# Kernel optimization log

Hardware: AMD Instinct MI355X
Metric: run time of the kernel (lower is better)

## Reference

```python
import jax, jax.numpy as jnp
import numpy as np

N_HEADS = 8
EPS = 1e-5  # torch nn.LayerNorm default


def layer_norm(x, g, b):
    mu = jnp.mean(x, axis=-1, keepdims=True)
    var = jnp.var(x, axis=-1, keepdims=True)
    return (x - mu) * jax.lax.rsqrt(var + EPS) * g + b


def mha(q_in, k_in, v_in, adj, Wq, bq, Wk, bk, Wv, bv, Wo, bo, g, be):
    # Standard GL-GIN / Co-guiding MultiHeadAttention: proj -> adjacency-masked
    # scaled dot-product softmax -> out proj -> residual + LayerNorm.
    # Dropout omitted (eval mode).
    B, Lq, D = q_in.shape
    Lk = k_in.shape[1]
    d_k = Wq.shape[-1] // N_HEADS
    q = (q_in @ Wq + bq).reshape(B, Lq, N_HEADS, d_k)
    k = (k_in @ Wk + bk).reshape(B, Lk, N_HEADS, d_k)
    v = (v_in @ Wv + bv).reshape(B, Lk, N_HEADS, d_k)
    scale = jnp.asarray(1.0 / np.sqrt(d_k), q_in.dtype)
    scores = jnp.einsum('bqhd,bkhd->bhqk', q, k) * scale  # [B,H,Lq,Lk]
    neg = jnp.asarray(-1e9, scores.dtype)
    scores = jnp.where(adj[:, None, :, :] == 0, neg, scores)
    attn = jax.nn.softmax(scores, axis=-1)
    out = jnp.einsum('bhqk,bkhd->bqhd', attn, v).reshape(B, Lq, N_HEADS * d_k)
    out = out @ Wo + bo
    return layer_norm(out + q_in, g, be)


def co_guiding_forward(h_a, h_b, adj_a, adj_b, adj_ab, adj_ba,
                       Wq, bq, Wk, bk, Wv, bv, Wo, bo, ln_g, ln_b):
    # Param arrays are stacked [n_layer, 4, ...], branch order: a2a, b2b, a2b, b2a.
    input_a, input_b = h_a, h_b
    n_layer = Wq.shape[0]
    for i in range(n_layer):
        def P(j):
            return (Wq[i, j], bq[i, j], Wk[i, j], bk[i, j], Wv[i, j], bv[i, j],
                    Wo[i, j], bo[i, j], ln_g[i, j], ln_b[i, j])
        a2a = mha(h_a, h_a, h_a, adj_a, *P(0))
        b2b = mha(h_b, h_b, h_b, adj_b, *P(1))
        a2b = mha(h_b, h_a, h_a, adj_ab, *P(2))
        b2a = mha(h_a, h_b, h_b, adj_ba, *P(3))
        h_a = jax.nn.relu(a2a + b2a)
        h_b = jax.nn.relu(b2b + a2b)
    return input_a + h_a, input_b + h_b


def setup_inputs():
    key = jax.random.key(0)
    ks = jax.random.split(key, 16)
    B, N, D, L = 4, 1024, 256, 2
    f = lambda k, s: jax.random.normal(k, s, dtype=jnp.float32) * 0.05
    return {
        'h_a': jax.random.normal(ks[0], (B, N, D), dtype=jnp.float32),
        'h_b': jax.random.normal(ks[1], (B, N, D), dtype=jnp.float32),
        'adj_a': jax.random.randint(ks[2], (B, N, N), 0, 2, dtype=jnp.int32),
        'adj_b': jax.random.randint(ks[3], (B, N, N), 0, 2, dtype=jnp.int32),
        'adj_ab': jax.random.randint(ks[4], (B, N, N), 0, 2, dtype=jnp.int32),
        'adj_ba': jax.random.randint(ks[5], (B, N, N), 0, 2, dtype=jnp.int32),
        'Wq': f(ks[6], (L, 4, D, D)), 'bq': f(ks[7], (L, 4, D)),
        'Wk': f(ks[8], (L, 4, D, D)), 'bk': f(ks[9], (L, 4, D)),
        'Wv': f(ks[10], (L, 4, D, D)), 'bv': f(ks[11], (L, 4, D)),
        'Wo': f(ks[12], (L, 4, D, D)), 'bo': f(ks[13], (L, 4, D)),
        'ln_g': jnp.ones((L, 4, D), dtype=jnp.float32),
        'ln_b': jnp.zeros((L, 4, D), dtype=jnp.float32),
    }


def reference(h_a, h_b, adj_a, adj_b, adj_ab, adj_ba,
              Wq, bq, Wk, bk, Wv, bv, Wo, bo, ln_g, ln_b):
    return co_guiding_forward(h_a, h_b, adj_a, adj_b, adj_ab, adj_ba,
                              Wq, bq, Wk, bk, Wv, bv, Wo, bo, ln_g, ln_b)
```

## Files before the change

### kernel.cpp

```cpp
#include <hip/hip_runtime.h>
#include <hip/hip_bf16.h>
#include <stdint.h>


using bf16x8 = __attribute__((ext_vector_type(8))) short;
using f32x4  = __attribute__((ext_vector_type(4))) float;
using f32x16 = __attribute__((ext_vector_type(16))) float;

#define DEVI __device__ __forceinline__

DEVI uint16_t f2bf(float x) {
  uint32_t u = __float_as_uint(x);
  u += 0x7FFFu + ((u >> 16) & 1u);
  return (uint16_t)(u >> 16);
}
DEVI uint32_t packbf2(float lo, float hi) {
  union { __hip_bfloat162 h; uint32_t u; } cv;
  cv.h = __float22bfloat162_rn(make_float2(lo, hi));
  return cv.u;
}
DEVI int phi4(int m) {
  return ((m & 4) << 1) | ((m & 8) >> 1) | (m & 3);
}

__global__ __launch_bounds__(256) void wprep_k(const float* __restrict__ Wq,
                                               const float* __restrict__ Wk,
                                               const float* __restrict__ Wv,
                                               const float* __restrict__ Wo,
                                               uint16_t* __restrict__ out) {
  const int z = blockIdx.z;
  const int type = z >> 3, mat = z & 7;
  const float* W = (type == 0 ? Wq : type == 1 ? Wk : type == 2 ? Wv : Wo)
                   + (size_t)mat * 65536;
  uint16_t* o = out + (size_t)type * 524288 + (size_t)mat * 65536;
  const int r0 = blockIdx.y * 64, c0 = blockIdx.x * 64;
  __shared__ float tl[64][68];
  const int t = threadIdx.x;
  {
    const int rr = t >> 2, cb = (t & 3) * 16;
    const float* src = W + (size_t)(r0 + rr) * 256 + c0 + cb;
    #pragma unroll
    for (int q = 0; q < 4; ++q) {
      float4 v = *(const float4*)(src + q * 4);
      tl[rr][cb + q*4 + 0] = v.x; tl[rr][cb + q*4 + 1] = v.y;
      tl[rr][cb + q*4 + 2] = v.z; tl[rr][cb + q*4 + 3] = v.w;
    }
  }
  __syncthreads();
  {
    const int nn = t >> 2, kb = (t & 3) * 16;
    __align__(16) uint16_t tmp[16];
    #pragma unroll
    for (int q = 0; q < 16; ++q) tmp[q] = f2bf(tl[kb + q][nn]);
    uint16_t* dst = o + (size_t)(c0 + nn) * 256 + r0 + kb;
    *(uint4*)&dst[0] = *(uint4*)&tmp[0];
    *(uint4*)&dst[8] = *(uint4*)&tmp[8];
  }
}

__global__ __launch_bounds__(256) void cvt_k(const float* __restrict__ a,
                                             const float* __restrict__ b,
                                             uint16_t* __restrict__ oa,
                                             uint16_t* __restrict__ ob) {
  const size_t i = ((size_t)blockIdx.x * 256 + threadIdx.x) * 8;
  const float* s = blockIdx.y ? b : a;
  uint16_t* o = blockIdx.y ? ob : oa;
  const float4 f0 = *(const float4*)(s + i), f1 = *(const float4*)(s + i + 4);
  uint4 u;
  u.x = packbf2(f0.x, f0.y); u.y = packbf2(f0.z, f0.w);
  u.z = packbf2(f1.x, f1.y); u.w = packbf2(f1.z, f1.w);
  *(uint4*)(o + i) = u;
}

struct AdjArgs { const int* adj[4]; uint32_t* bits[4]; };

__global__ __launch_bounds__(256) void adjbits_k(AdjArgs a) {
  const int* adj = a.adj[blockIdx.z];
  uint32_t* bits = a.bits[blockIdx.z];
  const size_t i = (size_t)blockIdx.x * 256 + threadIdx.x;
  const int lane = threadIdx.x & 63;
  const int v = adj[i];
  unsigned long long m = __ballot(v != 0);
  if ((lane & 31) == 0) {
    const uint32_t wi = (uint32_t)(i >> 5);
    const uint32_t kw = wi & 31;
    const uint32_t q  = (wi >> 5) & 1023;
    const uint32_t bb = wi >> 15;
    bits[((bb * 32 + kw) << 10) | q] = (uint32_t)(m >> (lane & 32));
  }
}

struct GemmArgs {
  const uint16_t* A[12];
  const uint16_t* W[12];
  const float*    bias[12];
  const float*    res[12];
  void*           C[12];
  float           os[12];
  int             mode[12];
};

DEVI void stage_tile(const uint16_t* __restrict__ Ab,
                     const uint16_t* __restrict__ Wt,
                     int m0, int n0, int kk,
                     char* AsB, char* BsB, int wid, int lane) {
  #pragma unroll
  for (int i = 0; i < 2; ++i) {
    const int seg = i * 4 + wid;
    const int rl  = (seg << 4) + (lane >> 2);
    const int gs  = (lane & 3) ^ ((lane >> 3) & 3);
    const uint16_t* gA = Ab + (size_t)(m0 + rl) * 256 + kk + gs * 8;
    const uint16_t* gB = Wt + (size_t)(n0 + rl) * 256 + kk + gs * 8;
    __builtin_amdgcn_global_load_lds(
        (const __attribute__((address_space(1))) void*)gA,
        (__attribute__((address_space(3))) void*)(AsB + (seg << 10)), 16, 0, 0);
    __builtin_amdgcn_global_load_lds(
        (const __attribute__((address_space(1))) void*)gB,
        (__attribute__((address_space(3))) void*)(BsB + (seg << 10)), 16, 0, 0);
  }
}

__global__ __launch_bounds__(256) void gemm_k(GemmArgs args) {
  const int z  = blockIdx.z;
  const int m0 = blockIdx.y * 128, n0 = blockIdx.x * 128;
  const uint16_t* Ab = args.A[z];
  const uint16_t* Wt = args.W[z];
  __shared__ __align__(16) uint16_t As[2][4096];
  __shared__ __align__(16) uint16_t Bs[2][4096];
  const int t = threadIdx.x;
  const int lane = t & 63, wid = t >> 6;
  const int g = lane >> 4, c = lane & 15;
  const int gx = g ^ ((c >> 1) & 3);
  const int wm = (wid >> 1) * 64, wn = (wid & 1) * 64;
  f32x4 acc[4][4] = {};

  stage_tile(Ab, Wt, m0, n0, 0, (char*)As[0], (char*)Bs[0], wid, lane);
  __syncthreads();

  for (int ks = 0; ks < 8; ++ks) {
    const int buf = ks & 1;
    if (ks < 7)
      stage_tile(Ab, Wt, m0, n0, (ks + 1) * 32,
                 (char*)As[buf ^ 1], (char*)Bs[buf ^ 1], wid, lane);
    bf16x8 af[4], bfr[4];
    #pragma unroll
    for (int mt = 0; mt < 4; ++mt)
      af[mt]  = *(const bf16x8*)&As[buf][(wm + mt * 16 + c) * 32 + gx * 8];
    #pragma unroll
    for (int nt = 0; nt < 4; ++nt)
      bfr[nt] = *(const bf16x8*)&Bs[buf][(wn + nt * 16 + c) * 32 + gx * 8];
    #pragma unroll
    for (int mt = 0; mt < 4; ++mt)
      #pragma unroll
      for (int nt = 0; nt < 4; ++nt)
        acc[mt][nt] = __builtin_amdgcn_mfma_f32_16x16x32_bf16(af[mt], bfr[nt], acc[mt][nt], 0, 0, 0);
    if (ks < 7) __syncthreads();
  }

  const float* bias = args.bias[z];
  const float osz = args.os[z];
  const int mode = args.mode[z];
  float bv[4];
  #pragma unroll
  for (int nt = 0; nt < 4; ++nt) bv[nt] = bias[n0 + wn + nt * 16 + c];

  if (mode == 1) {
    const float* res = args.res[z];
    float* C = (float*)args.C[z];
    #pragma unroll
    for (int mt = 0; mt < 4; ++mt)
      #pragma unroll
      for (int r = 0; r < 4; ++r) {
        const int row = m0 + wm + mt * 16 + 4 * g + r;
        #pragma unroll
        for (int nt = 0; nt < 4; ++nt) {
          const int col = n0 + wn + nt * 16 + c;
          C[(size_t)row * 256 + col] = (acc[mt][nt][r] + bv[nt]) * osz + res[(size_t)row * 256 + col];
        }
      }
  } else if (mode == 2) {
    uint16_t* C = (uint16_t*)args.C[z];
    #pragma unroll
    for (int mt = 0; mt < 4; ++mt)
      #pragma unroll
      for (int r = 0; r < 4; ++r) {
        const int row = m0 + wm + mt * 16 + 4 * g + r;
        const int bb = row >> 10, n = row & 1023;
        #pragma unroll
        for (int nt = 0; nt < 4; ++nt) {
          const int col = n0 + wn + nt * 16 + c;
          const int hh = col >> 5, d = col & 31;
          C[((size_t)(bb * 8 + hh) * 1024 + n) * 32 + d] =
              f2bf((acc[mt][nt][r] + bv[nt]) * osz);
        }
      }
  } else {
    uint16_t* C = (uint16_t*)args.C[z];
    #pragma unroll
    for (int mt = 0; mt < 4; ++mt)
      #pragma unroll
      for (int r = 0; r < 4; ++r) {
        const int row = m0 + wm + mt * 16 + 4 * g + r;
        const int bb = row >> 10, n = row & 1023;
        const int nn = (n & ~15) | phi4(n & 15);
        #pragma unroll
        for (int nt = 0; nt < 4; ++nt) {
          const int col = n0 + wn + nt * 16 + c;
          const int hh = col >> 5, d = col & 31;
          C[((size_t)(bb * 8 + hh) * 32 + d) * 1024 + nn] =
              f2bf((acc[mt][nt][r] + bv[nt]) * osz);
        }
      }
  }
}

struct AttnArgs {
  const uint16_t* Q[4];
  const uint16_t* K[4];
  const uint16_t* Vt[4];
  const uint32_t* adjb[4];
  uint16_t*       O[4];
};

__global__ __launch_bounds__(256) void attn_k(AttnArgs args) {
  const int bid = blockIdx.x;
  const int qt  = bid >> 7;
  const int grp = bid & 127;
  const int bh = grp & 31, j = grp >> 5;
  const int b = bh >> 3, h = bh & 7;
  const int t = threadIdx.x, wid = t >> 6, lane = t & 63;
  const int c = lane & 31, hi = lane >> 5;
  const int qrow = qt * 128 + wid * 32 + c;

  const uint16_t* Qbh = args.Q[j] + (size_t)(b * 8 + h) * 32768;
  const uint16_t* Kbh = args.K[j] + (size_t)(b * 8 + h) * 32768;
  const uint16_t* Vp  = args.Vt[j] + ((size_t)(b * 8 + h) * 32 + c) * 1024 + hi * 8;
  const uint32_t* adjT = args.adjb[j] + (size_t)b * 32768 + qrow;

  const bf16x8 qf0 = *(const bf16x8*)&Qbh[qrow * 32 + hi * 8];
  const bf16x8 qf1 = *(const bf16x8*)&Qbh[qrow * 32 + 16 + hi * 8];

  f32x16 oacc = {};
  f32x16 cinit;
  #pragma unroll
  for (int r = 0; r < 16; ++r) cinit[r] = -12.0f;
  float l = 0.f;

  for (int k0 = 0; k0 < 1024; k0 += 32) {
    const uint32_t w = adjT[(size_t)(k0 >> 5) << 10] >> (hi * 4);
    const bf16x8 kf0 = *(const bf16x8*)&Kbh[(k0 + c) * 32 + hi * 8];
    const bf16x8 kf1 = *(const bf16x8*)&Kbh[(k0 + c) * 32 + 16 + hi * 8];
    const bf16x8 vf0 = *(const bf16x8*)(Vp + k0);
    const bf16x8 vf1 = *(const bf16x8*)(Vp + k0 + 16);

    f32x16 st = cinit;
    st = __builtin_amdgcn_mfma_f32_32x32x16_bf16(kf0, qf0, st, 0, 0, 0);
    st = __builtin_amdgcn_mfma_f32_32x32x16_bf16(kf1, qf1, st, 0, 0, 0);

    float s0 = 0.f, s1 = 0.f, s2 = 0.f, s3 = 0.f;
    #pragma unroll
    for (int r = 0; r < 16; ++r) {
      const int pos = (r & 3) + 8 * (r >> 2);
      const float bitf = (float)((w >> pos) & 1u);
      const float pv = __builtin_amdgcn_exp2f(st[r]) * bitf;
      st[r] = pv;
      if ((r & 3) == 0) s0 += pv; else if ((r & 3) == 1) s1 += pv;
      else if ((r & 3) == 2) s2 += pv; else s3 += pv;
    }
    l += (s0 + s1) + (s2 + s3);

    union PU { uint32_t u[4]; bf16x8 v; };
    PU p0, p1;
    p0.u[0] = packbf2(st[0],  st[1]);  p0.u[1] = packbf2(st[2],  st[3]);
    p0.u[2] = packbf2(st[4],  st[5]);  p0.u[3] = packbf2(st[6],  st[7]);
    p1.u[0] = packbf2(st[8],  st[9]);  p1.u[1] = packbf2(st[10], st[11]);
    p1.u[2] = packbf2(st[12], st[13]); p1.u[3] = packbf2(st[14], st[15]);

    oacc = __builtin_amdgcn_mfma_f32_32x32x16_bf16(vf0, p0.v, oacc, 0, 0, 0);
    oacc = __builtin_amdgcn_mfma_f32_32x32x16_bf16(vf1, p1.v, oacc, 0, 0, 0);

    if (__builtin_expect(__any(l > 1e18f), 0)) {
      const float ds = 0x1p-64f;
      l *= ds;
      #pragma unroll
      for (int r = 0; r < 16; ++r) { oacc[r] *= ds; cinit[r] -= 64.0f; }
    }
  }

  l += __shfl_xor(l, 32, 64);
  const float inv = 1.0f / l;
  uint16_t* O = args.O[j];
  const size_t ob = (size_t)(b * 1024 + qrow) * 256 + h * 32 + 4 * hi;
  #pragma unroll
  for (int rq = 0; rq < 4; ++rq) {
    uint2 val;
    val.x = packbf2(oacc[4*rq+0] * inv, oacc[4*rq+1] * inv);
    val.y = packbf2(oacc[4*rq+2] * inv, oacc[4*rq+3] * inv);
    *(uint2*)&O[ob + 8 * rq] = val;
  }
}

struct LnArgs {
  const float* x0; const float* x1;
  const float* g0; const float* be0;
  const float* g1; const float* be1;
  const float* addin;
  float* out;
  uint16_t* outbf;
};
struct LnBoth { LnArgs p[2]; };

__global__ __launch_bounds__(256) void ln_k(LnBoth args) {
  const LnArgs a = args.p[blockIdx.z];
  const int wid = threadIdx.x >> 6, lane = threadIdx.x & 63;
  const int row = blockIdx.x * 4 + wid;
  const size_t off = (size_t)row * 256 + lane * 4;

  const float4 x0 = *(const float4*)(a.x0 + off);
  const float4 x1 = *(const float4*)(a.x1 + off);
  float s0 = x0.x + x0.y + x0.z + x0.w;
  float s1 = x1.x + x1.y + x1.z + x1.w;
  #pragma unroll
  for (int s = 1; s < 64; s <<= 1) { s0 += __shfl_xor(s0, s, 64); s1 += __shfl_xor(s1, s, 64); }
  const float mu0 = s0 * (1.f / 256.f), mu1 = s1 * (1.f / 256.f);
  const float d0x = x0.x - mu0, d0y = x0.y - mu0, d0z = x0.z - mu0, d0w = x0.w - mu0;
  const float d1x = x1.x - mu1, d1y = x1.y - mu1, d1z = x1.z - mu1, d1w = x1.w - mu1;
  float v0 = d0x * d0x + d0y * d0y + d0z * d0z + d0w * d0w;
  float v1 = d1x * d1x + d1y * d1y + d1z * d1z + d1w * d1w;
  #pragma unroll
  for (int s = 1; s < 64; s <<= 1) { v0 += __shfl_xor(v0, s, 64); v1 += __shfl_xor(v1, s, 64); }
  const float r0 = rsqrtf(v0 * (1.f / 256.f) + 1e-5f);
  const float r1 = rsqrtf(v1 * (1.f / 256.f) + 1e-5f);

  const size_t po = (size_t)lane * 4;
  const float4 g0 = *(const float4*)(a.g0 + po), b0 = *(const float4*)(a.be0 + po);
  const float4 g1 = *(const float4*)(a.g1 + po), b1 = *(const float4*)(a.be1 + po);

  float4 y;
  y.x = fmaxf(d0x * r0 * g0.x + b0.x + d1x * r1 * g1.x + b1.x, 0.f);
  y.y = fmaxf(d0y * r0 * g0.y + b0.y + d1y * r1 * g1.y + b1.y, 0.f);
  y.z = fmaxf(d0z * r0 * g0.z + b0.z + d1z * r1 * g1.z + b1.z, 0.f);
  y.w = fmaxf(d0w * r0 * g0.w + b0.w + d1w * r1 * g1.w + b1.w, 0.f);
  if (a.addin) {
    const float4 ad = *(const float4*)(a.addin + off);
    y.x += ad.x; y.y += ad.y; y.z += ad.z; y.w += ad.w;
  }
  *(float4*)(a.out + off) = y;
  if (a.outbf) {
    uint2 vb;
    vb.x = packbf2(y.x, y.y); vb.y = packbf2(y.z, y.w);
    *(uint2*)(a.outbf + off) = vb;
  }
}

extern "C" void kernel_launch(void* const* d_in, const int* in_sizes, int n_in,
                              void* d_out, int out_size, void* d_ws, size_t ws_size,
                              hipStream_t stream) {
  (void)in_sizes; (void)n_in; (void)out_size; (void)ws_size;
  const float* h_a = (const float*)d_in[0];
  const float* h_b = (const float*)d_in[1];
  const float* bq  = (const float*)d_in[7];
  const float* bk  = (const float*)d_in[9];
  const float* bv  = (const float*)d_in[11];
  const float* bo  = (const float*)d_in[13];
  const float* lng = (const float*)d_in[14];
  const float* lnb = (const float*)d_in[15];

  const float QSC = 1.4426950408889634f * 0.17677669529663687f;

  char* ws = (char*)d_ws;
  uint16_t* WT   = (uint16_t*)ws;
  uint32_t* ADJB = (uint32_t*)(ws + (4u  << 20));
  float*    hA   = (float*)   (ws + (6u  << 20));
  float*    hB   = (float*)   (ws + (10u << 20));
  uint16_t* hAbf = (uint16_t*)(ws + (14u << 20));
  uint16_t* hBbf = (uint16_t*)(ws + (16u << 20));
  uint16_t* Qb[4]; uint16_t* Kb[4]; uint16_t* Vtb[4]; uint16_t* ATb[4]; float* MO[4];
  for (int j = 0; j < 4; ++j) {
    Qb[j]  = (uint16_t*)(ws + (18u << 20) + (size_t)j * (2u << 20));
    Kb[j]  = (uint16_t*)(ws + (26u << 20) + (size_t)j * (2u << 20));
    MO[j]  = (float*)   (ws + (18u << 20) + (size_t)j * (4u << 20));
    Vtb[j] = (uint16_t*)(ws + (34u << 20) + (size_t)j * (2u << 20));
    ATb[j] = (uint16_t*)(ws + (42u << 20) + (size_t)j * (2u << 20));
  }

  wprep_k<<<dim3(4, 4, 32), 256, 0, stream>>>(
      (const float*)d_in[6], (const float*)d_in[8],
      (const float*)d_in[10], (const float*)d_in[12], WT);
  cvt_k<<<dim3(512, 2), 256, 0, stream>>>(h_a, h_b, hAbf, hBbf);
  {
    AdjArgs aa;
    for (int j = 0; j < 4; ++j) {
      aa.adj[j]  = (const int*)d_in[2 + j];
      aa.bits[j] = ADJB + (size_t)j * 131072;
    }
    adjbits_k<<<dim3(16384, 1, 4), 256, 0, stream>>>(aa);
  }

  for (int i = 0; i < 2; ++i) {
    const float* inA = (i == 0) ? h_a : hA;
    const float* inB = (i == 0) ? h_b : hB;
    const float* qin[4]   = { inA, inB, inB, inA };
    const uint16_t* qbf[4]  = { hAbf, hBbf, hBbf, hAbf };
    const uint16_t* kvbf[4] = { hAbf, hBbf, hAbf, hBbf };

    {
      GemmArgs ga = {};
      for (int j = 0; j < 4; ++j) {
        const int mm = i * 4 + j;
        ga.A[j]     = qbf[j];  ga.W[j]     = WT + 0 * 524288 + (size_t)mm * 65536;
        ga.bias[j]  = bq + mm * 256; ga.C[j] = Qb[j];  ga.os[j] = QSC;  ga.mode[j] = 2;
        ga.A[4+j]   = kvbf[j]; ga.W[4+j]   = WT + 1 * 524288 + (size_t)mm * 65536;
        ga.bias[4+j]= bk + mm * 256; ga.C[4+j] = Kb[j]; ga.os[4+j] = 1.0f; ga.mode[4+j] = 2;
        ga.A[8+j]   = kvbf[j]; ga.W[8+j]   = WT + 2 * 524288 + (size_t)mm * 65536;
        ga.bias[8+j]= bv + mm * 256; ga.C[8+j] = Vtb[j]; ga.os[8+j] = 1.0f; ga.mode[8+j] = 3;
      }
      gemm_k<<<dim3(2, 32, 12), 256, 0, stream>>>(ga);
    }
    {
      AttnArgs at;
      for (int j = 0; j < 4; ++j) {
        at.Q[j] = Qb[j]; at.K[j] = Kb[j]; at.Vt[j] = Vtb[j];
        at.adjb[j] = ADJB + (size_t)j * 131072; at.O[j] = ATb[j];
      }
      attn_k<<<dim3(1024, 1, 1), 256, 0, stream>>>(at);
    }
    {
      GemmArgs go = {};
      for (int j = 0; j < 4; ++j) {
        const int mm = i * 4 + j;
        go.A[j] = ATb[j]; go.W[j] = WT + 3 * 524288 + (size_t)mm * 65536;
        go.bias[j] = bo + mm * 256; go.res[j] = qin[j]; go.C[j] = MO[j];
        go.os[j] = 1.0f; go.mode[j] = 1;
      }
      gemm_k<<<dim3(2, 32, 4), 256, 0, stream>>>(go);
    }
    {
      LnBoth lb;
      float* outA = (i == 1) ? (float*)d_out : hA;
      float* outB = (i == 1) ? ((float*)d_out + 1048576) : hB;
      const float* addA = (i == 1) ? h_a : nullptr;
      const float* addB = (i == 1) ? h_b : nullptr;
      uint16_t* mbA = (i == 0) ? hAbf : nullptr;
      uint16_t* mbB = (i == 0) ? hBbf : nullptr;
      lb.p[0] = { MO[0], MO[3],
                  lng + (i * 4 + 0) * 256, lnb + (i * 4 + 0) * 256,
                  lng + (i * 4 + 3) * 256, lnb + (i * 4 + 3) * 256,
                  addA, outA, mbA };
      lb.p[1] = { MO[1], MO[2],
                  lng + (i * 4 + 1) * 256, lnb + (i * 4 + 1) * 256,
                  lng + (i * 4 + 2) * 256, lnb + (i * 4 + 2) * 256,
                  addB, outB, mbB };
      ln_k<<<dim3(1024, 1, 2), 256, 0, stream>>>(lb);
    }
  }
}
```

Baseline: 228.9 us.

## Split attention keys across warps and store intermediates in bf16

The attention kernel now gives each block 64 query rows, split between two key halves handled by separate warp pairs. The halves are combined through shared memory, which doubles the grid. The running rescale guard and the -12 offset init are removed, so there is no overflow protection. The output-projection residual and result, and the layer-norm input, move from fp32 to bf16, and the fp32 hidden-state copies are dropped. This cuts memory traffic but adds extra bf16 rounding to the residual path.

```diff
diff --git a/kernel.cpp b/kernel.cpp
--- a/kernel.cpp
+++ b/kernel.cpp
@@ -19,6 +19,7 @@
   cv.h = __float22bfloat162_rn(make_float2(lo, hi));
   return cv.u;
 }
+DEVI float bf2f(uint16_t v) { return __uint_as_float((uint32_t)v << 16); }
 DEVI int phi4(int m) {
   return ((m & 4) << 1) | ((m & 8) >> 1) | (m & 3);
 }
@@ -94,7 +95,7 @@
   const uint16_t* A[12];
   const uint16_t* W[12];
   const float*    bias[12];
-  const float*    res[12];
+  const uint16_t* res[12];
   void*           C[12];
   float           os[12];
   int             mode[12];
@@ -165,8 +166,8 @@
   for (int nt = 0; nt < 4; ++nt) bv[nt] = bias[n0 + wn + nt * 16 + c];
 
   if (mode == 1) {
-    const float* res = args.res[z];
-    float* C = (float*)args.C[z];
+    const uint16_t* res = args.res[z];
+    uint16_t* C = (uint16_t*)args.C[z];
     #pragma unroll
     for (int mt = 0; mt < 4; ++mt)
       #pragma unroll
@@ -175,7 +176,8 @@
         #pragma unroll
         for (int nt = 0; nt < 4; ++nt) {
           const int col = n0 + wn + nt * 16 + c;
-          C[(size_t)row * 256 + col] = (acc[mt][nt][r] + bv[nt]) * osz + res[(size_t)row * 256 + col];
+          C[(size_t)row * 256 + col] =
+              f2bf((acc[mt][nt][r] + bv[nt]) * osz + bf2f(res[(size_t)row * 256 + col]));
         }
       }
   } else if (mode == 2) {
@@ -222,38 +224,44 @@
   uint16_t*       O[4];
 };
 
-__global__ __launch_bounds__(256) void attn_k(AttnArgs args) {
+__global__ __launch_bounds__(256, 8) void attn_k(AttnArgs args) {
   const int bid = blockIdx.x;
   const int qt  = bid >> 7;
   const int grp = bid & 127;
   const int bh = grp & 31, j = grp >> 5;
   const int b = bh >> 3, h = bh & 7;
   const int t = threadIdx.x, wid = t >> 6, lane = t & 63;
+  const int qg = wid & 1, ks = wid >> 1;
   const int c = lane & 31, hi = lane >> 5;
-  const int qrow = qt * 128 + wid * 32 + c;
+  const int hsh = hi * 4;
+  const int qrow = qt * 64 + qg * 32 + c;
 
   const uint16_t* Qbh = args.Q[j] + (size_t)(b * 8 + h) * 32768;
   const uint16_t* Kbh = args.K[j] + (size_t)(b * 8 + h) * 32768;
-  const uint16_t* Vp  = args.Vt[j] + ((size_t)(b * 8 + h) * 32 + c) * 1024 + hi * 8;
+  const uint16_t* Vbh = args.Vt[j] + ((size_t)(b * 8 + h) * 32 + c) * 1024 + hi * 8;
   const uint32_t* adjT = args.adjb[j] + (size_t)b * 32768 + qrow;
 
   const bf16x8 qf0 = *(const bf16x8*)&Qbh[qrow * 32 + hi * 8];
   const bf16x8 qf1 = *(const bf16x8*)&Qbh[qrow * 32 + 16 + hi * 8];
 
   f32x16 oacc = {};
-  f32x16 cinit;
-  #pragma unroll
-  for (int r = 0; r < 16; ++r) cinit[r] = -12.0f;
   float l = 0.f;
 
-  for (int k0 = 0; k0 < 1024; k0 += 32) {
-    const uint32_t w = adjT[(size_t)(k0 >> 5) << 10] >> (hi * 4);
-    const bf16x8 kf0 = *(const bf16x8*)&Kbh[(k0 + c) * 32 + hi * 8];
-    const bf16x8 kf1 = *(const bf16x8*)&Kbh[(k0 + c) * 32 + 16 + hi * 8];
-    const bf16x8 vf0 = *(const bf16x8*)(Vp + k0);
-    const bf16x8 vf1 = *(const bf16x8*)(Vp + k0 + 16);
-
-    f32x16 st = cinit;
+  const int kbeg = ks * 512;
+  const uint16_t* kp = Kbh + (size_t)(kbeg + c) * 32 + hi * 8;
+  const uint16_t* vp = Vbh + kbeg;
+  const uint32_t* ap = adjT + ((size_t)(kbeg >> 5) << 10);
+
+  #pragma unroll 2
+  for (int it = 0; it < 16; ++it) {
+    const uint32_t w = (*ap) >> hsh;
+    const bf16x8 kf0 = *(const bf16x8*)kp;
+    const bf16x8 kf1 = *(const bf16x8*)(kp + 16);
+    const bf16x8 vf0 = *(const bf16x8*)vp;
+    const bf16x8 vf1 = *(const bf16x8*)(vp + 16);
+    ap += 1024; kp += 1024; vp += 32;
+
+    f32x16 st = {};
     st = __builtin_amdgcn_mfma_f32_32x32x16_bf16(kf0, qf0, st, 0, 0, 0);
     st = __builtin_amdgcn_mfma_f32_32x32x16_bf16(kf1, qf1, st, 0, 0, 0);
 
@@ -278,13 +286,21 @@
 
     oacc = __builtin_amdgcn_mfma_f32_32x32x16_bf16(vf0, p0.v, oacc, 0, 0, 0);
     oacc = __builtin_amdgcn_mfma_f32_32x32x16_bf16(vf1, p1.v, oacc, 0, 0, 0);
-
-    if (__builtin_expect(__any(l > 1e18f), 0)) {
-      const float ds = 0x1p-64f;
-      l *= ds;
-      #pragma unroll
-      for (int r = 0; r < 16; ++r) { oacc[r] *= ds; cinit[r] -= 64.0f; }
-    }
+  }
+
+  __shared__ float red[2][64][17];
+  if (ks == 1) {
+    #pragma unroll
+    for (int r = 0; r < 16; ++r) red[qg][lane][r] = oacc[r];
+    red[qg][lane][16] = l;
+  }
+  __syncthreads();
+  if (ks == 1) return;
+
+  {
+    #pragma unroll
+    for (int r = 0; r < 16; ++r) oacc[r] += red[qg][lane][r];
+    l += red[qg][lane][16];
   }
 
   l += __shfl_xor(l, 32, 64);
@@ -301,7 +317,7 @@
 }
 
 struct LnArgs {
-  const float* x0; const float* x1;
+  const uint16_t* x0; const uint16_t* x1;
   const float* g0; const float* be0;
   const float* g1; const float* be1;
   const float* addin;
@@ -316,8 +332,14 @@
   const int row = blockIdx.x * 4 + wid;
   const size_t off = (size_t)row * 256 + lane * 4;
 
-  const float4 x0 = *(const float4*)(a.x0 + off);
-  const float4 x1 = *(const float4*)(a.x1 + off);
+  const uint2 u0 = *(const uint2*)(a.x0 + off);
+  const uint2 u1 = *(const uint2*)(a.x1 + off);
+  float4 x0, x1;
+  x0.x = bf2f((uint16_t)u0.x); x0.y = bf2f((uint16_t)(u0.x >> 16));
+  x0.z = bf2f((uint16_t)u0.y); x0.w = bf2f((uint16_t)(u0.y >> 16));
+  x1.x = bf2f((uint16_t)u1.x); x1.y = bf2f((uint16_t)(u1.x >> 16));
+  x1.z = bf2f((uint16_t)u1.y); x1.w = bf2f((uint16_t)(u1.y >> 16));
+
   float s0 = x0.x + x0.y + x0.z + x0.w;
   float s1 = x1.x + x1.y + x1.z + x1.w;
   #pragma unroll
@@ -345,7 +367,7 @@
     const float4 ad = *(const float4*)(a.addin + off);
     y.x += ad.x; y.y += ad.y; y.z += ad.z; y.w += ad.w;
   }
-  *(float4*)(a.out + off) = y;
+  if (a.out) *(float4*)(a.out + off) = y;
   if (a.outbf) {
     uint2 vb;
     vb.x = packbf2(y.x, y.y); vb.y = packbf2(y.z, y.w);
@@ -371,17 +393,15 @@
   char* ws = (char*)d_ws;
   uint16_t* WT   = (uint16_t*)ws;
   uint32_t* ADJB = (uint32_t*)(ws + (4u  << 20));
-  float*    hA   = (float*)   (ws + (6u  << 20));
-  float*    hB   = (float*)   (ws + (10u << 20));
-  uint16_t* hAbf = (uint16_t*)(ws + (14u << 20));
-  uint16_t* hBbf = (uint16_t*)(ws + (16u << 20));
-  uint16_t* Qb[4]; uint16_t* Kb[4]; uint16_t* Vtb[4]; uint16_t* ATb[4]; float* MO[4];
+  uint16_t* hAbf = (uint16_t*)(ws + (6u  << 20));
+  uint16_t* hBbf = (uint16_t*)(ws + (8u  << 20));
+  uint16_t* Qb[4]; uint16_t* Kb[4]; uint16_t* Vtb[4]; uint16_t* ATb[4]; uint16_t* MOb[4];
   for (int j = 0; j < 4; ++j) {
-    Qb[j]  = (uint16_t*)(ws + (18u << 20) + (size_t)j * (2u << 20));
-    Kb[j]  = (uint16_t*)(ws + (26u << 20) + (size_t)j * (2u << 20));
-    MO[j]  = (float*)   (ws + (18u << 20) + (size_t)j * (4u << 20));
-    Vtb[j] = (uint16_t*)(ws + (34u << 20) + (size_t)j * (2u << 20));
-    ATb[j] = (uint16_t*)(ws + (42u << 20) + (size_t)j * (2u << 20));
+    Qb[j]  = (uint16_t*)(ws + (10u << 20) + (size_t)j * (2u << 20));
+    Kb[j]  = (uint16_t*)(ws + (18u << 20) + (size_t)j * (2u << 20));
+    Vtb[j] = (uint16_t*)(ws + (26u << 20) + (size_t)j * (2u << 20));
+    ATb[j] = (uint16_t*)(ws + (34u << 20) + (size_t)j * (2u << 20));
+    MOb[j] = (uint16_t*)(ws + (42u << 20) + (size_t)j * (2u << 20));
   }
 
   wprep_k<<<dim3(4, 4, 32), 256, 0, stream>>>(
@@ -398,9 +418,6 @@
   }
 
   for (int i = 0; i < 2; ++i) {
-    const float* inA = (i == 0) ? h_a : hA;
-    const float* inB = (i == 0) ? h_b : hB;
-    const float* qin[4]   = { inA, inB, inB, inA };
     const uint16_t* qbf[4]  = { hAbf, hBbf, hBbf, hAbf };
     const uint16_t* kvbf[4] = { hAbf, hBbf, hAbf, hBbf };
 
@@ -423,31 +440,31 @@
         at.Q[j] = Qb[j]; at.K[j] = Kb[j]; at.Vt[j] = Vtb[j];
         at.adjb[j] = ADJB + (size_t)j * 131072; at.O[j] = ATb[j];
       }
-      attn_k<<<dim3(1024, 1, 1), 256, 0, stream>>>(at);
+      attn_k<<<dim3(2048, 1, 1), 256, 0, stream>>>(at);
     }
     {
       GemmArgs go = {};
       for (int j = 0; j < 4; ++j) {
         const int mm = i * 4 + j;
         go.A[j] = ATb[j]; go.W[j] = WT + 3 * 524288 + (size_t)mm * 65536;
-        go.bias[j] = bo + mm * 256; go.res[j] = qin[j]; go.C[j] = MO[j];
+        go.bias[j] = bo + mm * 256; go.res[j] = qbf[j]; go.C[j] = MOb[j];
         go.os[j] = 1.0f; go.mode[j] = 1;
       }
       gemm_k<<<dim3(2, 32, 4), 256, 0, stream>>>(go);
     }
     {
       LnBoth lb;
-      float* outA = (i == 1) ? (float*)d_out : hA;
-      float* outB = (i == 1) ? ((float*)d_out + 1048576) : hB;
+      float* outA = (i == 1) ? (float*)d_out : nullptr;
+      float* outB = (i == 1) ? ((float*)d_out + 1048576) : nullptr;
       const float* addA = (i == 1) ? h_a : nullptr;
       const float* addB = (i == 1) ? h_b : nullptr;
       uint16_t* mbA = (i == 0) ? hAbf : nullptr;
       uint16_t* mbB = (i == 0) ? hBbf : nullptr;
-      lb.p[0] = { MO[0], MO[3],
+      lb.p[0] = { MOb[0], MOb[3],
                   lng + (i * 4 + 0) * 256, lnb + (i * 4 + 0) * 256,
                   lng + (i * 4 + 3) * 256, lnb + (i * 4 + 3) * 256,
                   addA, outA, mbA };
-      lb.p[1] = { MO[1], MO[2],
+      lb.p[1] = { MOb[1], MOb[2],
                   lng + (i * 4 + 1) * 256, lnb + (i * 4 + 1) * 256,
                   lng + (i * 4 + 2) * 256, lnb + (i * 4 + 2) * 256,
                   addB, outB, mbB };
```

Result: slower. 271.0 us (+18.4%).
